# Optimization experiments

Measured on AMD Instinct MI355X. Metric: run time of the kernel, lower is better.

The kernel has to match this reference:

```python
import jax, jax.numpy as jnp
import numpy as np

S, B, D = 1024, 2, 1024      # seq, batch, embed_dim
E, TOPK = 15, 3              # routed experts = 8*2-1, top_n = 2*2-1
F = 1024                     # per-expert ffn dim (ffn_dim // m)
FS = 2048                    # shared expert ffn dim (ffn_dim * n_shared)


def _uinit(k, shape, out_dim):
    std = out_dim ** -0.5
    return jax.random.uniform(k, shape, jnp.float32, -std, std)


def setup_inputs() -> dict:
    key = jax.random.key(0)
    ks = jax.random.split(key, 10)
    return {
        "x": jax.random.normal(ks[0], (S, B, D), jnp.float32),
        "gate_w": jax.random.normal(ks[1], (E, D), jnp.float32) * (D ** -0.5),
        "fc1_w": _uinit(ks[2], (E, 2 * F, D), 2 * F),
        "fc1_b": _uinit(ks[3], (E, 2 * F), 2 * F),
        "geglu_mult": jnp.ones((E, F), jnp.float32),
        "fc2_w": _uinit(ks[4], (E, D, F), D),
        "fc2_b": _uinit(ks[5], (E, D), D),
        "s_fc1_w": _uinit(ks[6], (2 * FS, D), 2 * FS),
        "s_fc1_b": _uinit(ks[7], (2 * FS,), 2 * FS),
        "s_geglu_mult": jnp.ones((FS,), jnp.float32),
        "s_fc2_w": _uinit(ks[8], (D, FS), D),
        "s_fc2_b": _uinit(ks[9], (D,), D),
    }


def reference(x, gate_w, fc1_w, fc1_b, geglu_mult, fc2_w, fc2_b,
              s_fc1_w, s_fc1_b, s_geglu_mult, s_fc2_w, s_fc2_b):
    s, b, d = x.shape
    xt = x.reshape(-1, d)                              # [T, D] tokens
    T = xt.shape[0]

    # --- gate: softmax over routed experts, top-k, renormalize ---
    logits = xt @ gate_w.T                             # [T, E]
    scores = jax.nn.softmax(logits, axis=-1)
    topk_w, topk_idx = jax.lax.top_k(scores, TOPK)     # [T, K]
    topk_w = topk_w / (jnp.sum(topk_w, axis=-1, keepdims=True) + 1e-20)
    # combine weights: zero for non-routed experts (same math as dispatch/scatter)
    comb = jnp.zeros((T, E), xt.dtype).at[jnp.arange(T)[:, None], topk_idx].add(topk_w)

    # --- routed experts: GEGLU FFN applied as grouped GEMM, weighted combine ---
    h = jnp.einsum('td,efd->etf', xt, fc1_w) + fc1_b[:, None, :]   # [E, T, 2F]
    xh, g = h[..., :F], h[..., F:]                                 # chunk: (x, gate)
    a = jax.nn.gelu(g, approximate=False) * xh * geglu_mult[:, None, :]
    yexp = jnp.einsum('etf,edf->etd', a, fc2_w) + fc2_b[:, None, :]  # [E, T, D]
    y = jnp.einsum('etd,te->td', yexp, comb)                         # [T, D]

    # --- shared expert ---
    hs = xt @ s_fc1_w.T + s_fc1_b                      # [T, 2*FS]
    xs, gs = hs[..., :FS], hs[..., FS:]
    as_ = jax.nn.gelu(gs, approximate=False) * xs * s_geglu_mult
    ys = as_ @ s_fc2_w.T + s_fc2_b                     # [T, D]

    return (y + ys).reshape(s, b, d)
```

## Files before the change

### kernel.cpp

```cpp
#include <hip/hip_runtime.h>

typedef __attribute__((ext_vector_type(8))) short bfrag;
typedef __attribute__((ext_vector_type(4))) float f32x4;

__device__ __forceinline__ short f2bf(float f) {
  union { float f; unsigned u; } v; v.f = f;
  unsigned r = v.u + 0x7FFFu + ((v.u >> 16) & 1u);
  return (short)(r >> 16);
}
__device__ __forceinline__ float bf2f(unsigned short h) {
  union { unsigned u; float f; } v; v.u = ((unsigned)h) << 16;
  return v.f;
}
__device__ __forceinline__ float gelu_exact(float g) {
  return 0.5f * g * (1.0f + erff(g * 0.70710678118654752f));
}
__device__ __forceinline__ void gld_lds16(const short* g, short* l) {
  __builtin_amdgcn_global_load_lds(
      (const __attribute__((address_space(1))) void*)g,
      (__attribute__((address_space(3))) void*)l, 16, 0, 0);
}

__global__ __launch_bounds__(256) void k_convert_w(
    const float* __restrict__ s0, const float* __restrict__ s1,
    const float* __restrict__ s2, const float* __restrict__ s3,
    short* __restrict__ d0, short* __restrict__ d1,
    short* __restrict__ d2, short* __restrict__ d3)
{
  const int b = blockIdx.x;
  const float* s; short* d; long off;
  if (b < 1920)      { s = s0; d = d0; off = (long)b * 4096; }
  else if (b < 2880) { s = s1; d = d1; off = (long)(b - 1920) * 4096; }
  else if (b < 3136) { s = s2; d = d2; off = (long)(b - 2880) * 4096; }
  else               { s = s3; d = d3; off = (long)(b - 3136) * 4096; }
#pragma unroll
  for (int j = 0; j < 16; j++) {
    const long i = off + j * 256 + threadIdx.x;
    const float4 v = ((const float4*)s)[i];
    ((short4*)d)[i] = make_short4(f2bf(v.x), f2bf(v.y), f2bf(v.z), f2bf(v.w));
  }
}

__global__ __launch_bounds__(64) void k_gate(const float* __restrict__ x,
    const float* __restrict__ gw, int* __restrict__ topk_idx,
    float* __restrict__ topk_w, short* __restrict__ xbf)
{
  const int t0 = blockIdx.x * 4;
  const int lane = threadIdx.x;
  float xv[4][16];
#pragma unroll
  for (int tt = 0; tt < 4; tt++)
#pragma unroll
    for (int i = 0; i < 16; i++) {
      xv[tt][i] = x[(size_t)(t0 + tt) * 1024 + lane + 64 * i];
      xbf[(size_t)(t0 + tt) * 1024 + lane + 64 * i] = f2bf(xv[tt][i]);
    }
  float p[4][15];
#pragma unroll
  for (int e = 0; e < 15; e++) {
    float wv[16];
#pragma unroll
    for (int i = 0; i < 16; i++) wv[i] = gw[(size_t)e * 1024 + lane + 64 * i];
#pragma unroll
    for (int tt = 0; tt < 4; tt++) {
      float s = 0.f;
#pragma unroll
      for (int i = 0; i < 16; i++) s += xv[tt][i] * wv[i];
#pragma unroll
      for (int o = 32; o; o >>= 1) s += __shfl_xor(s, o, 64);
      p[tt][e] = s;
    }
  }
#pragma unroll
  for (int tt = 0; tt < 4; tt++) {
    float m = -1e30f;
#pragma unroll
    for (int e = 0; e < 15; e++) m = fmaxf(m, p[tt][e]);
    float q[15], Z = 0.f;
#pragma unroll
    for (int e = 0; e < 15; e++) { q[e] = expf(p[tt][e] - m); Z += q[e]; }
    int usedMask = 0; int bi[3]; float bv[3];
#pragma unroll
    for (int j = 0; j < 3; j++) {
      float best = -1.f; int b = 0;
#pragma unroll
      for (int e = 0; e < 15; e++) {
        bool ok = (!((usedMask >> e) & 1)) && (q[e] > best);
        if (ok) { best = q[e]; b = e; }
      }
      bi[j] = b; bv[j] = best / Z; usedMask |= 1 << b;
    }
    if (lane == tt) {
      float den = bv[0] + bv[1] + bv[2] + 1e-20f;
#pragma unroll
      for (int j = 0; j < 3; j++) {
        topk_idx[(t0 + tt) * 3 + j] = bi[j];
        topk_w[(t0 + tt) * 3 + j] = bv[j] / den;
      }
    }
  }
}

__global__ __launch_bounds__(1024) void k_route(const int* __restrict__ topk_idx,
    const float* __restrict__ topk_w, int* __restrict__ cnt_g, int* __restrict__ offs_g,
    int* __restrict__ row_tok, float* __restrict__ row_wt, int* __restrict__ row_id)
{
  __shared__ int scnt[16], soffs[16], sfill[16];
  const int tid = threadIdx.x;
  if (tid < 16) { scnt[tid] = 0; sfill[tid] = 0; }
  __syncthreads();
  for (int i = tid; i < 6144; i += 1024) atomicAdd(&scnt[topk_idx[i]], 1);
  __syncthreads();
  if (tid == 0) {
    int a = 0;
    for (int e = 0; e < 15; e++) { soffs[e] = a; offs_g[e] = a; cnt_g[e] = scnt[e]; a += scnt[e]; }
  }
  __syncthreads();
  for (int i = tid; i < 6144; i += 1024) {
    int e = topk_idx[i];
    int pos = atomicAdd(&sfill[e], 1);
    int row = soffs[e] + pos;
    row_tok[row] = i / 3;
    row_wt[row] = topk_w[i];
    row_id[i] = row;
  }
}

__device__ __forceinline__ bool resolve_tile128(const int* __restrict__ cnt, int ty,
                                                int& e, int& lt) {
  int acc = 0;
#pragma unroll
  for (int i = 0; i < 15; i++) {
    int tl = (cnt[i] + 127) >> 7;
    if (ty < acc + tl) { e = i; lt = ty - acc; return true; }
    acc += tl;
  }
  return false;
}

__global__ __launch_bounds__(256) void k_fc1(
    const short* __restrict__ xbf,
    const short* __restrict__ wsh, const float* __restrict__ bsh, const float* __restrict__ msh,
    const short* __restrict__ wex, const float* __restrict__ bex, const float* __restrict__ mex,
    const int* __restrict__ cnt, const int* __restrict__ offs, const int* __restrict__ row_tok,
    short* __restrict__ as_buf, short* __restrict__ a_buf)
{
  __shared__ short smem[2 * 128 * 64];
  short* As = smem;
  short* Bs = smem + 128 * 64;
  const int tid = threadIdx.x;
  const int bid = blockIdx.x;
  const bool sh = bid < 512;
  int f0, m0 = 0, e = 0, rowBase = 0, nrows = 128;
  if (sh) {
    f0 = (bid & 31) * 64; m0 = (bid >> 5) * 128;
  } else {
    const int b2 = bid - 512;
    int lt;
    if (!resolve_tile128(cnt, b2 >> 4, e, lt)) return;
    f0 = (b2 & 15) * 64;
    rowBase = offs[e] + lt * 128;
    nrows = cnt[e] - lt * 128; if (nrows > 128) nrows = 128;
  }
  const int lane = tid & 63, ml = lane & 15, kq = lane >> 4, mlo = lane & 7;
  const int wv = tid >> 6, wr = wv >> 1, wc = wv & 1;
  const int lrow = lane >> 3, lchk = lane & 7;
  const int Fhalf = sh ? 2048 : 1024;
  const short* wptr = sh ? wsh : (wex + (size_t)e * 2048 * 1024);
  const short* aSrc[4]; const short* bSrc[4];
#pragma unroll
  for (int t = 0; t < 4; t++) {
    const int r = wv * 32 + t * 8 + lrow;
    const int sc = (lchk ^ (r & 7)) * 8;
    if (sh) aSrc[t] = xbf + (size_t)(m0 + r) * 1024 + sc;
    else {
      const int rc = r < nrows ? r : nrows - 1;
      aSrc[t] = xbf + (size_t)row_tok[rowBase + rc] * 1024 + sc;
    }
    const int grow = (r < 64) ? (f0 + r) : (Fhalf + f0 + r - 64);
    bSrc[t] = wptr + (size_t)grow * 1024 + sc;
  }
  f32x4 acc[4][4] = {};
  for (int k0 = 0; k0 < 1024; k0 += 64) {
#pragma unroll
    for (int t = 0; t < 4; t++) gld_lds16(aSrc[t] + k0, As + (wv * 32 + t * 8) * 64);
#pragma unroll
    for (int t = 0; t < 4; t++) gld_lds16(bSrc[t] + k0, Bs + (wv * 32 + t * 8) * 64);
    __syncthreads();
#pragma unroll
    for (int kk = 0; kk < 2; kk++) {
      const int so = ((kk * 4 + kq) ^ mlo) * 8;
      bfrag af[4], bf[4];
#pragma unroll
      for (int i = 0; i < 4; i++) af[i] = *(bfrag*)&As[(wr * 64 + i * 16 + ml) * 64 + so];
#pragma unroll
      for (int j = 0; j < 4; j++) {
        const int brow = ((j >> 1) ? 64 : 0) + wc * 32 + (j & 1) * 16 + ml;
        bf[j] = *(bfrag*)&Bs[brow * 64 + so];
      }
#pragma unroll
      for (int i = 0; i < 4; i++)
#pragma unroll
        for (int j = 0; j < 4; j++)
          acc[i][j] = __builtin_amdgcn_mfma_f32_16x16x32_bf16(af[i], bf[j], acc[i][j], 0, 0, 0);
    }
    __syncthreads();
  }
  const float* bias = sh ? bsh : (bex + (size_t)e * 2048);
  const float* mult = sh ? msh : (mex + (size_t)e * 1024);
#pragma unroll
  for (int jj = 0; jj < 2; jj++) {
    const int fl = wc * 32 + jj * 16 + ml;
    const int f = f0 + fl;
    const float b1 = bias[f];
    const float b2 = bias[Fhalf + f];
    const float mv = mult[f];
#pragma unroll
    for (int i = 0; i < 4; i++)
#pragma unroll
      for (int rg = 0; rg < 4; rg++) {
        const int row = wr * 64 + i * 16 + kq * 4 + rg;
        const float h1 = acc[i][jj][rg] + b1;
        const float h2 = acc[i][jj + 2][rg] + b2;
        const short o = f2bf(gelu_exact(h2) * h1 * mv);
        if (sh) as_buf[(size_t)(m0 + row) * 2048 + f] = o;
        else if (row < nrows) a_buf[(size_t)(rowBase + row) * 1024 + f] = o;
      }
  }
}

__global__ __launch_bounds__(256) void k_fc2(
    const short* __restrict__ as_buf, const short* __restrict__ wsfc2, const float* __restrict__ s_b,
    const short* __restrict__ a_buf, const short* __restrict__ wfc2, const float* __restrict__ e_b,
    const int* __restrict__ cnt, const int* __restrict__ offs, const float* __restrict__ row_wt,
    float* __restrict__ y, short* __restrict__ yexp)
{
  __shared__ short smem[2 * 128 * 64];
  short* As = smem;
  short* Bs = smem + 128 * 64;
  const int tid = threadIdx.x;
  const int bid = blockIdx.x;
  const bool sh = bid < 128;
  int d0, m0 = 0, e = 0, rowBase = 0, nrows = 128, Klen, astr, bstr;
  const short *aBase, *bBase;
  if (sh) {
    d0 = (bid & 7) * 128; m0 = (bid >> 3) * 128;
    Klen = 2048; astr = 2048; bstr = 2048;
    aBase = as_buf; bBase = wsfc2;
  } else {
    const int b2 = bid - 128;
    int lt;
    if (!resolve_tile128(cnt, b2 >> 3, e, lt)) return;
    d0 = (b2 & 7) * 128;
    rowBase = offs[e] + lt * 128;
    nrows = cnt[e] - lt * 128; if (nrows > 128) nrows = 128;
    Klen = 1024; astr = 1024; bstr = 1024;
    aBase = a_buf + (size_t)rowBase * 1024;
    bBase = wfc2 + (size_t)e * 1024 * 1024;
  }
  const int lane = tid & 63, ml = lane & 15, kq = lane >> 4, mlo = lane & 7;
  const int wv = tid >> 6, wr = wv >> 1, wc = wv & 1;
  const int lrow = lane >> 3, lchk = lane & 7;
  const short* aSrc[4]; const short* bSrc[4];
#pragma unroll
  for (int t = 0; t < 4; t++) {
    const int r = wv * 32 + t * 8 + lrow;
    const int sc = (lchk ^ (r & 7)) * 8;
    aSrc[t] = aBase + (size_t)(sh ? (m0 + r) : r) * astr + sc;
    bSrc[t] = bBase + (size_t)(d0 + r) * bstr + sc;
  }
  f32x4 acc[4][4] = {};
  for (int k0 = 0; k0 < Klen; k0 += 64) {
#pragma unroll
    for (int t = 0; t < 4; t++) gld_lds16(aSrc[t] + k0, As + (wv * 32 + t * 8) * 64);
#pragma unroll
    for (int t = 0; t < 4; t++) gld_lds16(bSrc[t] + k0, Bs + (wv * 32 + t * 8) * 64);
    __syncthreads();
#pragma unroll
    for (int kk = 0; kk < 2; kk++) {
      const int so = ((kk * 4 + kq) ^ mlo) * 8;
      bfrag af[4], bf[4];
#pragma unroll
      for (int i = 0; i < 4; i++) af[i] = *(bfrag*)&As[(wr * 64 + i * 16 + ml) * 64 + so];
#pragma unroll
      for (int j = 0; j < 4; j++) bf[j] = *(bfrag*)&Bs[(wc * 64 + j * 16 + ml) * 64 + so];
#pragma unroll
      for (int i = 0; i < 4; i++)
#pragma unroll
        for (int j = 0; j < 4; j++)
          acc[i][j] = __builtin_amdgcn_mfma_f32_16x16x32_bf16(af[i], bf[j], acc[i][j], 0, 0, 0);
    }
    __syncthreads();
  }
#pragma unroll
  for (int j = 0; j < 4; j++) {
    const int d = d0 + wc * 64 + j * 16 + ml;
    const float bv = sh ? s_b[d] : e_b[(size_t)e * 1024 + d];
#pragma unroll
    for (int i = 0; i < 4; i++)
#pragma unroll
      for (int rg = 0; rg < 4; rg++) {
        const int row = wr * 64 + i * 16 + kq * 4 + rg;
        if (sh) {
          y[(size_t)(m0 + row) * 1024 + d] = acc[i][j][rg] + bv;
        } else if (row < nrows) {
          const float wt = row_wt[rowBase + row];
          yexp[(size_t)(rowBase + row) * 1024 + d] = f2bf((acc[i][j][rg] + bv) * wt);
        }
      }
  }
}

__global__ __launch_bounds__(256) void k_combine(float* __restrict__ y,
    const short* __restrict__ yexp, const int* __restrict__ row_id)
{
  const int idx = blockIdx.x * 256 + threadIdx.x;
  const int t = idx >> 8;
  const int d4 = (idx & 255) * 4;
  const int r0 = row_id[t * 3], r1 = row_id[t * 3 + 1], r2 = row_id[t * 3 + 2];
  float4 acc = *(float4*)(y + (size_t)t * 1024 + d4);
  const ushort4 v0 = *(const ushort4*)(yexp + (size_t)r0 * 1024 + d4);
  const ushort4 v1 = *(const ushort4*)(yexp + (size_t)r1 * 1024 + d4);
  const ushort4 v2 = *(const ushort4*)(yexp + (size_t)r2 * 1024 + d4);
  acc.x += bf2f(v0.x) + bf2f(v1.x) + bf2f(v2.x);
  acc.y += bf2f(v0.y) + bf2f(v1.y) + bf2f(v2.y);
  acc.z += bf2f(v0.z) + bf2f(v1.z) + bf2f(v2.z);
  acc.w += bf2f(v0.w) + bf2f(v1.w) + bf2f(v2.w);
  *(float4*)(y + (size_t)t * 1024 + d4) = acc;
}

extern "C" void kernel_launch(void* const* d_in, const int* in_sizes, int n_in,
                              void* d_out, int out_size, void* d_ws, size_t ws_size,
                              hipStream_t stream) {
  const float* x          = (const float*)d_in[0];
  const float* gate_w     = (const float*)d_in[1];
  const float* fc1_w      = (const float*)d_in[2];
  const float* fc1_b      = (const float*)d_in[3];
  const float* geglu_mult = (const float*)d_in[4];
  const float* fc2_w      = (const float*)d_in[5];
  const float* fc2_b      = (const float*)d_in[6];
  const float* s_fc1_w    = (const float*)d_in[7];
  const float* s_fc1_b    = (const float*)d_in[8];
  const float* s_mult     = (const float*)d_in[9];
  const float* s_fc2_w    = (const float*)d_in[10];
  const float* s_fc2_b    = (const float*)d_in[11];
  float* y = (float*)d_out;

  char* wsb = (char*)d_ws;
  int*   cnt      = (int*)(wsb + 0);
  int*   offs     = (int*)(wsb + 64);
  int*   topk_idx = (int*)(wsb + 256);
  float* topk_w   = (float*)(wsb + 24832);
  int*   row_tok  = (int*)(wsb + 49408);
  float* row_wt   = (float*)(wsb + 74496);
  int*   row_id   = (int*)(wsb + 99584);
  short* xbf      = (short*)(wsb + 131072);
  short* a_buf    = (short*)(wsb + 8519680);
  short* as_buf   = (short*)(wsb + 21364736);
  short* yexp     = (short*)(wsb + 29753344);
  short* wbf_sfc1 = (short*)(wsb + 42598400);
  short* wbf_sfc2 = (short*)(wsb + 50987008);
  short* wbf_fc1  = (short*)(wsb + 55181312);
  short* wbf_fc2  = (short*)(wsb + 118095872);

  k_convert_w<<<3264, 256, 0, stream>>>(fc1_w, fc2_w, s_fc1_w, s_fc2_w,
                                        wbf_fc1, wbf_fc2, wbf_sfc1, wbf_sfc2);
  k_gate<<<512, 64, 0, stream>>>(x, gate_w, topk_idx, topk_w, xbf);
  k_route<<<1, 1024, 0, stream>>>(topk_idx, topk_w, cnt, offs, row_tok, row_wt, row_id);
  k_fc1<<<1520, 256, 0, stream>>>(xbf, wbf_sfc1, s_fc1_b, s_mult,
                                  wbf_fc1, fc1_b, geglu_mult,
                                  cnt, offs, row_tok, as_buf, a_buf);
  k_fc2<<<632, 256, 0, stream>>>(as_buf, wbf_sfc2, s_fc2_b,
                                 a_buf, wbf_fc2, fc2_b,
                                 cnt, offs, row_wt, y, yexp);
  k_combine<<<2048, 256, 0, stream>>>(y, yexp, row_id);
}
```

Baseline: 458.2 us.

## Fuse expert combine into fc2 via atomic adds and split weight conversion blocks

Result: slower. 489.0 us (+6.7%).

```diff
diff --git a/kernel.cpp b/kernel.cpp
--- a/kernel.cpp
+++ b/kernel.cpp
@@ -29,16 +29,18 @@
 {
   const int b = blockIdx.x;
   const float* s; short* d; long off;
-  if (b < 1920)      { s = s0; d = d0; off = (long)b * 4096; }
-  else if (b < 2880) { s = s1; d = d1; off = (long)(b - 1920) * 4096; }
-  else if (b < 3136) { s = s2; d = d2; off = (long)(b - 2880) * 4096; }
-  else               { s = s3; d = d3; off = (long)(b - 3136) * 4096; }
-#pragma unroll
-  for (int j = 0; j < 16; j++) {
-    const long i = off + j * 256 + threadIdx.x;
-    const float4 v = ((const float4*)s)[i];
-    ((short4*)d)[i] = make_short4(f2bf(v.x), f2bf(v.y), f2bf(v.z), f2bf(v.w));
-  }
+  if (b < 3840)      { s = s0; d = d0; off = (long)b * 2048; }
+  else if (b < 5760) { s = s1; d = d1; off = (long)(b - 3840) * 2048; }
+  else if (b < 6272) { s = s2; d = d2; off = (long)(b - 5760) * 2048; }
+  else               { s = s3; d = d3; off = (long)(b - 6272) * 2048; }
+  const long base = off + threadIdx.x;
+  float4 v[8];
+#pragma unroll
+  for (int j = 0; j < 8; j++) v[j] = ((const float4*)s)[base + j * 256];
+#pragma unroll
+  for (int j = 0; j < 8; j++)
+    ((short4*)d)[base + j * 256] =
+        make_short4(f2bf(v[j].x), f2bf(v[j].y), f2bf(v[j].z), f2bf(v[j].w));
 }
 
 __global__ __launch_bounds__(64) void k_gate(const float* __restrict__ x,
@@ -232,8 +234,9 @@
 __global__ __launch_bounds__(256) void k_fc2(
     const short* __restrict__ as_buf, const short* __restrict__ wsfc2, const float* __restrict__ s_b,
     const short* __restrict__ a_buf, const short* __restrict__ wfc2, const float* __restrict__ e_b,
-    const int* __restrict__ cnt, const int* __restrict__ offs, const float* __restrict__ row_wt,
-    float* __restrict__ y, short* __restrict__ yexp)
+    const int* __restrict__ cnt, const int* __restrict__ offs,
+    const float* __restrict__ row_wt, const int* __restrict__ row_tok,
+    float* __restrict__ y)
 {
   __shared__ short smem[2 * 128 * 64];
   short* As = smem;
@@ -302,31 +305,14 @@
       for (int rg = 0; rg < 4; rg++) {
         const int row = wr * 64 + i * 16 + kq * 4 + rg;
         if (sh) {
-          y[(size_t)(m0 + row) * 1024 + d] = acc[i][j][rg] + bv;
+          atomicAdd(&y[(size_t)(m0 + row) * 1024 + d], acc[i][j][rg] + bv);
         } else if (row < nrows) {
           const float wt = row_wt[rowBase + row];
-          yexp[(size_t)(rowBase + row) * 1024 + d] = f2bf((acc[i][j][rg] + bv) * wt);
+          const int tok = row_tok[rowBase + row];
+          atomicAdd(&y[(size_t)tok * 1024 + d], (acc[i][j][rg] + bv) * wt);
         }
       }
   }
-}
-
-__global__ __launch_bounds__(256) void k_combine(float* __restrict__ y,
-    const short* __restrict__ yexp, const int* __restrict__ row_id)
-{
-  const int idx = blockIdx.x * 256 + threadIdx.x;
-  const int t = idx >> 8;
-  const int d4 = (idx & 255) * 4;
-  const int r0 = row_id[t * 3], r1 = row_id[t * 3 + 1], r2 = row_id[t * 3 + 2];
-  float4 acc = *(float4*)(y + (size_t)t * 1024 + d4);
-  const ushort4 v0 = *(const ushort4*)(yexp + (size_t)r0 * 1024 + d4);
-  const ushort4 v1 = *(const ushort4*)(yexp + (size_t)r1 * 1024 + d4);
-  const ushort4 v2 = *(const ushort4*)(yexp + (size_t)r2 * 1024 + d4);
-  acc.x += bf2f(v0.x) + bf2f(v1.x) + bf2f(v2.x);
-  acc.y += bf2f(v0.y) + bf2f(v1.y) + bf2f(v2.y);
-  acc.z += bf2f(v0.z) + bf2f(v1.z) + bf2f(v2.z);
-  acc.w += bf2f(v0.w) + bf2f(v1.w) + bf2f(v2.w);
-  *(float4*)(y + (size_t)t * 1024 + d4) = acc;
 }
 
 extern "C" void kernel_launch(void* const* d_in, const int* in_sizes, int n_in,
@@ -357,13 +343,13 @@
   short* xbf      = (short*)(wsb + 131072);
   short* a_buf    = (short*)(wsb + 8519680);
   short* as_buf   = (short*)(wsb + 21364736);
-  short* yexp     = (short*)(wsb + 29753344);
   short* wbf_sfc1 = (short*)(wsb + 42598400);
   short* wbf_sfc2 = (short*)(wsb + 50987008);
   short* wbf_fc1  = (short*)(wsb + 55181312);
   short* wbf_fc2  = (short*)(wsb + 118095872);
 
-  k_convert_w<<<3264, 256, 0, stream>>>(fc1_w, fc2_w, s_fc1_w, s_fc2_w,
+  hipMemsetAsync(y, 0, (size_t)2048 * 1024 * 4, stream);
+  k_convert_w<<<6528, 256, 0, stream>>>(fc1_w, fc2_w, s_fc1_w, s_fc2_w,
                                         wbf_fc1, wbf_fc2, wbf_sfc1, wbf_sfc2);
   k_gate<<<512, 64, 0, stream>>>(x, gate_w, topk_idx, topk_w, xbf);
   k_route<<<1, 1024, 0, stream>>>(topk_idx, topk_w, cnt, offs, row_tok, row_wt, row_id);
@@ -372,6 +358,5 @@
                                   cnt, offs, row_tok, as_buf, a_buf);
   k_fc2<<<632, 256, 0, stream>>>(as_buf, wbf_sfc2, s_fc2_b,
                                  a_buf, wbf_fc2, fc2_b,
-                                 cnt, offs, row_wt, y, yexp);
-  k_combine<<<2048, 256, 0, stream>>>(y, yexp, row_id);
-}
+                                 cnt, offs, row_wt, row_tok, y);
+}
```
